# Performance work log

Measured on AMD Instinct MI355X. Metric: run time of the kernel, lower is better.

The kernel has to match this reference:

```python
import jax, jax.numpy as jnp
import numpy as np

HEADS = 16
DIM_HEAD = 64
DIM = 1024
INNER = HEADS * DIM_HEAD  # 1024
DIM_OUT = 1024


def setup_inputs() -> dict:
    key = jax.random.key(0)
    k1, k2, k3, k4 = jax.random.split(key, 4)
    B, N = 4, 2048
    x = jax.random.normal(k1, (B, N, DIM), dtype=jnp.float32)
    # hk.Linear(inner_dim*3, with_bias=False): weight shape [in, out]
    w_qkv = jax.random.normal(k2, (DIM, INNER * 3), dtype=jnp.float32) / np.sqrt(DIM)
    # hk.Linear(dim_out): weight [INNER, DIM_OUT] + bias
    w_out = jax.random.normal(k3, (INNER, DIM_OUT), dtype=jnp.float32) / np.sqrt(INNER)
    b_out = jax.random.normal(k4, (DIM_OUT,), dtype=jnp.float32) * 0.01
    return {"x": x, "w_qkv": w_qkv, "w_out": w_out, "b_out": b_out}


def reference(x, w_qkv, w_out, b_out):
    B, N, _ = x.shape
    scale = DIM_HEAD ** -0.5
    qkv = x @ w_qkv  # [B, N, 3*INNER]
    q, k, v = jnp.split(qkv, 3, axis=-1)
    # b n (h d) -> b h n d
    split_heads = lambda t: t.reshape(B, N, HEADS, DIM_HEAD).transpose(0, 2, 1, 3)
    q, k, v = split_heads(q), split_heads(k), split_heads(v)
    dots = jnp.einsum('bhid,bhjd->bhij', q, k) * scale  # [B, H, N, N]
    attn = jax.nn.softmax(dots, axis=-1)
    out = jnp.einsum('bhij,bhjd->bhid', attn, v)  # [B, H, N, D]
    out = out.transpose(0, 2, 1, 3).reshape(B, N, INNER)  # b h n d -> b n (h d)
    return out @ w_out + b_out
```

## Files before the change

kernel.cpp:

```cpp
#include <hip/hip_runtime.h>
#include <cstdint>


typedef unsigned short ushort_t;
typedef _Float16 half_t;
typedef half_t half8 __attribute__((ext_vector_type(8)));
typedef half_t half4 __attribute__((ext_vector_type(4)));
typedef __fp16 fp16x2 __attribute__((ext_vector_type(2)));
typedef float floatx4 __attribute__((ext_vector_type(4)));

#define QSCALE 0.18033688011112043f

__device__ __forceinline__ float bf2f(ushort_t h) {
  union { unsigned int u; float f; } v; v.u = ((unsigned int)h) << 16; return v.f;
}
__device__ __forceinline__ void async_copy16(const void* g, void* l) {
  __builtin_amdgcn_global_load_lds(
      reinterpret_cast<const __attribute__((address_space(1))) unsigned int*>(
          reinterpret_cast<uintptr_t>(g)),
      reinterpret_cast<__attribute__((address_space(3))) unsigned int*>(
          reinterpret_cast<uintptr_t>(l)),
      16, 0, 0);
}
__device__ __forceinline__ void lds_fence() {
  asm volatile("s_waitcnt lgkmcnt(0)" ::: "memory");
}
__device__ __forceinline__ void vm_fence() {
  asm volatile("s_waitcnt vmcnt(0)" ::: "memory");
}

__global__ __launch_bounds__(256) void detect_dtype(const ushort_t* __restrict__ x,
                                                    int* __restrict__ flag) {
  __shared__ int cnt;
  if (threadIdx.x == 0) cnt = 0;
  __syncthreads();
  int local = 0;
  for (int i = threadIdx.x; i < 8192; i += 256)
    if ((x[i] & 0x7F80u) == 0x7F80u) ++local;
  atomicAdd(&cnt, local);
  __syncthreads();
  if (threadIdx.x == 0) *flag = (cnt >= 2) ? 1 : 0;
}

__global__ __launch_bounds__(256) void convert_to_f16(const void* __restrict__ src,
                                                      half_t* __restrict__ dst, int n,
                                                      const int* __restrict__ flag) {
  const int i0 = (blockIdx.x * 256 + threadIdx.x) * 4;
  if (i0 >= n) return;
  if (*flag) {
    const float* s = (const float*)src;
#pragma unroll
    for (int j = 0; j < 4; ++j) dst[i0 + j] = (half_t)s[i0 + j];
  } else {
    const ushort_t* s = (const ushort_t*)src;
#pragma unroll
    for (int j = 0; j < 4; ++j) dst[i0 + j] = (half_t)bf2f(s[i0 + j]);
  }
}

__global__ __launch_bounds__(256) void convert_bias(const void* __restrict__ src,
                                                    float* __restrict__ dst,
                                                    const int* __restrict__ flag) {
  const int i = blockIdx.x * 256 + threadIdx.x;
  if (i >= 1024) return;
  dst[i] = (*flag) ? ((const float*)src)[i] : bf2f(((const ushort_t*)src)[i]);
}

__global__ __launch_bounds__(256) void transpose_conv2(const void* __restrict__ srcA,
                                                       half_t* __restrict__ dstA,
                                                       const void* __restrict__ srcB,
                                                       half_t* __restrict__ dstB,
                                                       const int* __restrict__ flag) {
  __shared__ half_t tile[64][65];
  const int bx = blockIdx.x;
  const void* src; half_t* dst; int C, c0;
  if (bx < 48) { src = srcA; dst = dstA; C = 3072; c0 = bx * 64; }
  else         { src = srcB; dst = dstB; C = 1024; c0 = (bx - 48) * 64; }
  const int R = 1024;
  const int r0 = blockIdx.y * 64;
  const int tx = threadIdx.x & 63, ty = threadIdx.x >> 6;
  if (*flag) {
    const float* s = (const float*)src;
    for (int i = ty; i < 64; i += 4) tile[i][tx] = (half_t)s[(size_t)(r0 + i) * C + (c0 + tx)];
  } else {
    const ushort_t* s = (const ushort_t*)src;
    for (int i = ty; i < 64; i += 4) tile[i][tx] = (half_t)bf2f(s[(size_t)(r0 + i) * C + (c0 + tx)]);
  }
  __syncthreads();
  for (int i = ty; i < 64; i += 4) dst[(size_t)(c0 + i) * R + (r0 + tx)] = tile[tx][i];
}

__global__ __launch_bounds__(256) void gemm_qkv_kernel(
    const half_t* __restrict__ X, const half_t* __restrict__ WT,
    half_t* __restrict__ Qb, half_t* __restrict__ Kb, half_t* __restrict__ VTb) {
  __shared__ half_t smem[128 * 136];
  half_t* As = smem;
  half_t* Bs = smem + 128 * 64;
  const int tid = threadIdx.x;
  const int wv = tid >> 6, lane = tid & 63;
  const int l15 = lane & 15, quad = lane >> 4;
  const int l7 = l15 & 7;
  const int wm = wv & 1, wn = wv >> 1;
  const int bid = blockIdx.x;
  const int xcd = bid & 7, idx = bid >> 3;
  const int mb = xcd * 8 + (idx & 7);
  const int nb = idx >> 3;
  const int rlo = lane >> 3, ci = lane & 7;
  const int sw_klo = (ci ^ rlo) * 8;

  floatx4 acc[4][4];
  const floatx4 z = {0.f, 0.f, 0.f, 0.f};
#pragma unroll
  for (int mi = 0; mi < 4; ++mi)
#pragma unroll
    for (int ni = 0; ni < 4; ++ni) acc[mi][ni] = z;

  const half_t* Abase = X + (size_t)mb * 128 * 1024;
  const half_t* Bbase = WT + (size_t)nb * 128 * 1024;

  for (int k0 = 0; k0 < 1024; k0 += 64) {
#pragma unroll
    for (int j = 0; j < 4; ++j) {
      const int rb = (wv * 4 + j) * 8;
      async_copy16(Abase + (size_t)(rb + rlo) * 1024 + k0 + sw_klo, &As[rb * 64]);
    }
#pragma unroll
    for (int j = 0; j < 4; ++j) {
      const int rb = (wv * 4 + j) * 8;
      async_copy16(Bbase + (size_t)(rb + rlo) * 1024 + k0 + sw_klo, &Bs[rb * 64]);
    }
    __syncthreads();
#pragma unroll
    for (int ks = 0; ks < 2; ++ks) {
      half8 af[4], bfv[4];
#pragma unroll
      for (int mi = 0; mi < 4; ++mi) {
        const int rr = wm * 64 + mi * 16 + l15;
        af[mi] = *(const half8*)&As[rr * 64 + (((ks * 4 + quad) ^ l7) * 8)];
      }
#pragma unroll
      for (int ni = 0; ni < 4; ++ni) {
        const int rr = wn * 64 + ni * 16 + l15;
        bfv[ni] = *(const half8*)&Bs[rr * 64 + (((ks * 4 + quad) ^ l7) * 8)];
      }
#pragma unroll
      for (int mi = 0; mi < 4; ++mi)
#pragma unroll
        for (int ni = 0; ni < 4; ++ni)
          acc[mi][ni] = __builtin_amdgcn_mfma_f32_16x16x32_f16(af[mi], bfv[ni], acc[mi][ni], 0, 0, 0);
    }
    __syncthreads();
  }

  const int which = nb >> 3;
  if (which != 2) {
    const float sc = (which == 0) ? QSCALE : 1.0f;
#pragma unroll
    for (int mi = 0; mi < 4; ++mi)
#pragma unroll
      for (int ni = 0; ni < 4; ++ni) {
        const int col = wn * 64 + ni * 16 + l15;
#pragma unroll
        for (int r = 0; r < 4; ++r) {
          const int row = wm * 64 + mi * 16 + quad * 4 + r;
          smem[row * 132 + col] = (half_t)(acc[mi][ni][r] * sc);
        }
      }
    __syncthreads();
    half_t* dstB = (which == 0) ? Qb : Kb;
    const int hbase = (nb & 7) * 2;
    const int c2 = lane * 2;
    const int hh = hbase + (c2 >> 6);
    const int dd = c2 & 63;
#pragma unroll 4
    for (int i = 0; i < 32; ++i) {
      const int row = wv * 32 + i;
      const uint32_t val = *(const uint32_t*)&smem[row * 132 + c2];
      const int rowg = mb * 128 + row;
      const int bb = rowg >> 11, nn = rowg & 2047;
      *(uint32_t*)&dstB[(((size_t)(bb * 16 + hh)) * 2048 + nn) * 64 + dd] = val;
    }
  } else {
    const int nb2 = nb - 16;
#pragma unroll
    for (int mi = 0; mi < 4; ++mi)
#pragma unroll
      for (int ni = 0; ni < 4; ++ni) {
        const int nl = wn * 64 + ni * 16 + l15;
#pragma unroll
        for (int r = 0; r < 4; ++r) {
          const int ml = wm * 64 + mi * 16 + quad * 4 + r;
          smem[nl * 136 + ml] = (half_t)acc[mi][ni][r];
        }
      }
    __syncthreads();
    const int bb = mb >> 4;
    const int nn0 = (mb * 128) & 2047;
    const int lane2 = lane * 2;
#pragma unroll 4
    for (int it = 0; it < 32; ++it) {
      const int row = it * 4 + wv;
      const int hh = nb2 * 2 + (row >> 6);
      const int dd = row & 63;
      const int keyoff = lane2 ^ ((dd & 8) ? 4 : 0);
      const uint32_t val = *(const uint32_t*)&smem[row * 136 + lane2];
      *(uint32_t*)&VTb[((size_t)((bb * 16 + hh) * 64 + dd)) * 2048 + nn0 + keyoff] = val;
    }
  }
}

__global__ __launch_bounds__(512) void attn_kernel(
    const half_t* __restrict__ Qb, const half_t* __restrict__ Kb,
    const half_t* __restrict__ VTb, half_t* __restrict__ Ob) {
  __shared__ half_t smem[16384];
  const int tid = threadIdx.x, wv = tid >> 6, lane = tid & 63;
  const int l15 = lane & 15, quad = lane >> 4;
  const int l7 = l15 & 7;
  const int bid = blockIdx.x;
  const int xcd = bid & 7, idx = bid >> 3;
  const int bh = ((idx & 7) << 3) + xcd;
  const int qt = idx >> 3;
  const int bq = bh >> 4, hh = bh & 15;
  const half_t* Qg = Qb + (size_t)bh * 2048 * 64;
  const half_t* Kg = Kb + (size_t)bh * 2048 * 64;
  const half_t* Vg = VTb + (size_t)bh * 64 * 2048;
  const int q0 = qt * 256;
  const int rlo = lane >> 3, ci = lane & 7;
  const int sw_klo = (ci ^ rlo) * 8;

  const int q1 = quad >> 1, qb0 = quad & 1, b3 = (l15 >> 3) & 1;
  int kx[2], vx[4];
#pragma unroll
  for (int ks = 0; ks < 2; ++ks) kx[ks] = ((ks * 4 + quad) ^ l7) * 8;
#pragma unroll
  for (int ki = 0; ki < 4; ++ki)
    vx[ki] = (((ki * 2 + q1) ^ l7) * 8) + ((qb0 ^ b3) * 4);

#pragma unroll
  for (int j = 0; j < 4; ++j) {
    const int rb = (wv * 4 + j) * 8;
    async_copy16(Qg + (size_t)(q0 + rb + rlo) * 64 + sw_klo, &smem[rb * 64]);
  }
  vm_fence();
  half8 aq[2][2];
#pragma unroll
  for (int ks = 0; ks < 2; ++ks)
#pragma unroll
    for (int qi = 0; qi < 2; ++qi) {
      const int rr = wv * 32 + qi * 16 + l15;
      aq[ks][qi] = *(const half8*)&smem[rr * 64 + (((ks * 4 + quad) ^ l7) * 8)];
    }
  __syncthreads();

  floatx4 o_acc[2][4];
  const floatx4 z = {0.f, 0.f, 0.f, 0.f};
  float l_st[2] = {0.f, 0.f};
#pragma unroll
  for (int qi = 0; qi < 2; ++qi)
#pragma unroll
    for (int di = 0; di < 4; ++di) o_acc[qi][di] = z;

  {
    const int rb = wv * 8;
    async_copy16(Kg + (size_t)(rb + rlo) * 64 + sw_klo, &smem[rb * 64]);
    async_copy16(Vg + (size_t)(rb + rlo) * 2048 + sw_klo, &smem[8192 + rb * 64]);
  }

#pragma unroll 2
  for (int t = 0; t < 32; ++t) {
    const int co = (t & 1) * 4096;
    const int po = 4096 - co;
    __syncthreads();
    if (t < 31) {
      const int rb = wv * 8;
      async_copy16(Kg + (size_t)((t + 1) * 64 + rb + rlo) * 64 + sw_klo,
                   &smem[po + rb * 64]);
      async_copy16(Vg + (size_t)(rb + rlo) * 2048 + (t + 1) * 64 + sw_klo,
                   &smem[8192 + po + rb * 64]);
    }
    const half_t* Kc = &smem[co];
    const half_t* Vc = &smem[8192 + co];

    floatx4 s_acc[4][2];
#pragma unroll
    for (int ki = 0; ki < 4; ++ki)
#pragma unroll
      for (int qi = 0; qi < 2; ++qi) s_acc[ki][qi] = z;
#pragma unroll
    for (int ks = 0; ks < 2; ++ks) {
      half8 bk[4];
#pragma unroll
      for (int ki = 0; ki < 4; ++ki)
        bk[ki] = *(const half8*)&Kc[(ki * 16 + l15) * 64 + kx[ks]];
      __builtin_amdgcn_s_setprio(1);
#pragma unroll
      for (int ki = 0; ki < 4; ++ki)
#pragma unroll
        for (int qi = 0; qi < 2; ++qi)
          s_acc[ki][qi] = __builtin_amdgcn_mfma_f32_16x16x32_f16(bk[ki], aq[ks][qi], s_acc[ki][qi], 0, 0, 0);
      __builtin_amdgcn_s_setprio(0);
    }

#pragma unroll
    for (int c = 0; c < 2; ++c) {
      half8 bv[4];
#pragma unroll
      for (int di = 0; di < 4; ++di) {
        union { half4 q[2]; half8 v; } b_;
        b_.q[0] = *(const half4*)&Vc[(di * 16 + l15) * 64 + vx[2 * c]];
        b_.q[1] = *(const half4*)&Vc[(di * 16 + l15) * 64 + vx[2 * c + 1]];
        bv[di] = b_.v;
      }
      union Ap { uint32_t u[4]; half8 h; } apu[2];
#pragma unroll
      for (int kii = 0; kii < 2; ++kii)
#pragma unroll
        for (int qi = 0; qi < 2; ++qi) {
          const int ki = c * 2 + kii;
          const float p0 = __builtin_amdgcn_exp2f(s_acc[ki][qi][0]);
          const float p1 = __builtin_amdgcn_exp2f(s_acc[ki][qi][1]);
          const float p2 = __builtin_amdgcn_exp2f(s_acc[ki][qi][2]);
          const float p3 = __builtin_amdgcn_exp2f(s_acc[ki][qi][3]);
          l_st[qi] += (p0 + p1) + (p2 + p3);
          union { fp16x2 v; uint32_t u; } lo_, hi_;
          lo_.v = __builtin_amdgcn_cvt_pkrtz(p0, p1);
          hi_.v = __builtin_amdgcn_cvt_pkrtz(p2, p3);
          apu[qi].u[kii * 2] = lo_.u;
          apu[qi].u[kii * 2 + 1] = hi_.u;
        }
      __builtin_amdgcn_s_setprio(1);
#pragma unroll
      for (int qi = 0; qi < 2; ++qi)
#pragma unroll
        for (int di = 0; di < 4; ++di)
          o_acc[qi][di] = __builtin_amdgcn_mfma_f32_16x16x32_f16(apu[qi].h, bv[di], o_acc[qi][di], 0, 0, 0);
      __builtin_amdgcn_s_setprio(0);
    }
  }

  float linv[2];
#pragma unroll
  for (int qi = 0; qi < 2; ++qi) {
    float rs = l_st[qi];
    rs += __shfl_xor(rs, 16);
    rs += __shfl_xor(rs, 32);
    linv[qi] = 1.0f / rs;
  }

  __syncthreads();
  const int c2 = (tid & 31) * 2;
  const int rbase = (tid >> 5) & 15;
#pragma unroll
  for (int p = 0; p < 2; ++p) {
    if ((wv >> 2) == p) {
      const int rw = (wv & 3) * 32;
#pragma unroll
      for (int qi = 0; qi < 2; ++qi)
#pragma unroll
        for (int r = 0; r < 4; ++r) {
          const float inv = __shfl(linv[qi], quad * 4 + r);
          const int rowl = rw + qi * 16 + quad * 4 + r;
#pragma unroll
          for (int di = 0; di < 4; ++di)
            smem[rowl * 72 + di * 16 + l15] = (half_t)(o_acc[qi][di][r] * inv);
        }
    }
    __syncthreads();
#pragma unroll 4
    for (int i = 0; i < 8; ++i) {
      const int rowl = i * 16 + rbase;
      const uint32_t val = *(const uint32_t*)&smem[rowl * 72 + c2];
      const int nn = q0 + p * 128 + rowl;
      *(uint32_t*)&Ob[((size_t)(bq * 2048 + nn)) * 1024 + hh * 64 + c2] = val;
    }
    __syncthreads();
  }
}

__global__ __launch_bounds__(256) void gemm_out_kernel(
    const half_t* __restrict__ A, const half_t* __restrict__ WT,
    const float* __restrict__ bias, float* __restrict__ out) {
  __shared__ half_t As[128 * 64];
  __shared__ half_t Bs[128 * 64];
  const int tid = threadIdx.x;
  const int wv = tid >> 6, lane = tid & 63;
  const int l15 = lane & 15, quad = lane >> 4;
  const int l7 = l15 & 7;
  const int wm = wv & 1, wn = wv >> 1;
  const int bid = blockIdx.x;
  const int xcd = bid & 7, idx = bid >> 3;
  const int mb = xcd * 8 + (idx & 7);
  const int nb = idx >> 3;
  const int rlo = lane >> 3, ci = lane & 7;
  const int sw_klo = (ci ^ rlo) * 8;

  floatx4 acc[4][4];
  const floatx4 z = {0.f, 0.f, 0.f, 0.f};
#pragma unroll
  for (int mi = 0; mi < 4; ++mi)
#pragma unroll
    for (int ni = 0; ni < 4; ++ni) acc[mi][ni] = z;

  const half_t* Abase = A + (size_t)mb * 128 * 1024;
  const half_t* Bbase = WT + (size_t)nb * 128 * 1024;

  for (int k0 = 0; k0 < 1024; k0 += 64) {
#pragma unroll
    for (int j = 0; j < 4; ++j) {
      const int rb = (wv * 4 + j) * 8;
      async_copy16(Abase + (size_t)(rb + rlo) * 1024 + k0 + sw_klo, &As[rb * 64]);
    }
#pragma unroll
    for (int j = 0; j < 4; ++j) {
      const int rb = (wv * 4 + j) * 8;
      async_copy16(Bbase + (size_t)(rb + rlo) * 1024 + k0 + sw_klo, &Bs[rb * 64]);
    }
    __syncthreads();
#pragma unroll
    for (int ks = 0; ks < 2; ++ks) {
      half8 af[4], bfv[4];
#pragma unroll
      for (int mi = 0; mi < 4; ++mi) {
        const int rr = wm * 64 + mi * 16 + l15;
        af[mi] = *(const half8*)&As[rr * 64 + (((ks * 4 + quad) ^ l7) * 8)];
      }
#pragma unroll
      for (int ni = 0; ni < 4; ++ni) {
        const int rr = wn * 64 + ni * 16 + l15;
        bfv[ni] = *(const half8*)&Bs[rr * 64 + (((ks * 4 + quad) ^ l7) * 8)];
      }
#pragma unroll
      for (int mi = 0; mi < 4; ++mi)
#pragma unroll
        for (int ni = 0; ni < 4; ++ni)
          acc[mi][ni] = __builtin_amdgcn_mfma_f32_16x16x32_f16(af[mi], bfv[ni], acc[mi][ni], 0, 0, 0);
    }
    __syncthreads();
  }

#pragma unroll
  for (int mi = 0; mi < 4; ++mi) {
#pragma unroll
    for (int ni = 0; ni < 4; ++ni) {
      const int colg = nb * 128 + wn * 64 + ni * 16 + l15;
      const float bs = bias[colg];
#pragma unroll
      for (int r = 0; r < 4; ++r) {
        const int rowg = mb * 128 + wm * 64 + mi * 16 + quad * 4 + r;
        out[(size_t)rowg * 1024 + colg] = acc[mi][ni][r] + bs;
      }
    }
  }
}

extern "C" void kernel_launch(void* const* d_in, const int* in_sizes, int n_in,
                              void* d_out, int out_size, void* d_ws, size_t ws_size,
                              hipStream_t stream) {
  const void* x_raw     = d_in[0];
  const void* w_qkv_raw = d_in[1];
  const void* w_out_raw = d_in[2];
  const void* b_out_raw = d_in[3];
  float* out = (float*)d_out;

  char* ws = (char*)d_ws;
  half_t* xb    = (half_t*)(ws);
  half_t* Qb    = (half_t*)(ws + ((size_t)16 << 20));
  half_t* Kb    = (half_t*)(ws + ((size_t)32 << 20));
  half_t* VTb   = (half_t*)(ws + ((size_t)48 << 20));
  half_t* WTqkv = (half_t*)(ws + ((size_t)64 << 20));
  half_t* WTout = (half_t*)(ws + ((size_t)70 << 20));
  float*  bb    = (float*)(ws + ((size_t)72 << 20));
  int*    flag  = (int*)(ws + ((size_t)72 << 20) + 8192);
  half_t* Ob    = xb;

  detect_dtype<<<1, 256, 0, stream>>>((const ushort_t*)x_raw, flag);
  convert_to_f16<<<8192, 256, 0, stream>>>(x_raw, xb, 8192 * 1024, flag);
  convert_bias<<<4, 256, 0, stream>>>(b_out_raw, bb, flag);
  transpose_conv2<<<dim3(64, 16), 256, 0, stream>>>(w_qkv_raw, WTqkv, w_out_raw, WTout, flag);
  gemm_qkv_kernel<<<1536, 256, 0, stream>>>(xb, WTqkv, Qb, Kb, VTb);
  attn_kernel<<<512, 512, 0, stream>>>(Qb, Kb, VTb, Ob);
  gemm_out_kernel<<<512, 256, 0, stream>>>(Ob, WTout, bb, out);
}
```

Baseline: 277.8 us.

## Use four-stage K/V LDS ring and process two tiles per barrier

Grows shared memory to hold four K/V tile buffers and restructures the main attention loop so each iteration processes two 64-key tiles after a single barrier, while prefetching the next two tiles. This halves the number of block-wide barriers and gives async loads more lead time to hide global latency. LDS use doubles to 64 KB per block, which may reduce occupancy. The scores still use exp2 with no running max, so the numerics are unchanged.

```diff
diff --git a/kernel.cpp b/kernel.cpp
--- a/kernel.cpp
+++ b/kernel.cpp
@@ -212,7 +212,7 @@
 __global__ __launch_bounds__(512) void attn_kernel(
     const half_t* __restrict__ Qb, const half_t* __restrict__ Kb,
     const half_t* __restrict__ VTb, half_t* __restrict__ Ob) {
-  __shared__ half_t smem[16384];
+  __shared__ half_t smem[32768];
   const int tid = threadIdx.x, wv = tid >> 6, lane = tid & 63;
   const int l15 = lane & 15, quad = lane >> 4;
   const int l7 = l15 & 7;
@@ -262,79 +262,91 @@
 
   {
     const int rb = wv * 8;
-    async_copy16(Kg + (size_t)(rb + rlo) * 64 + sw_klo, &smem[rb * 64]);
-    async_copy16(Vg + (size_t)(rb + rlo) * 2048 + sw_klo, &smem[8192 + rb * 64]);
+#pragma unroll
+    for (int u = 0; u < 2; ++u) {
+      async_copy16(Kg + (size_t)(u * 64 + rb + rlo) * 64 + sw_klo,
+                   &smem[u * 4096 + rb * 64]);
+      async_copy16(Vg + (size_t)(rb + rlo) * 2048 + u * 64 + sw_klo,
+                   &smem[16384 + u * 4096 + rb * 64]);
+    }
   }
 
 #pragma unroll 2
-  for (int t = 0; t < 32; ++t) {
-    const int co = (t & 1) * 4096;
-    const int po = 4096 - co;
-    __syncthreads();
-    if (t < 31) {
+  for (int t = 0; t < 32; t += 2) {
+    __syncthreads();
+    if (t < 30) {
       const int rb = wv * 8;
-      async_copy16(Kg + (size_t)((t + 1) * 64 + rb + rlo) * 64 + sw_klo,
-                   &smem[po + rb * 64]);
-      async_copy16(Vg + (size_t)(rb + rlo) * 2048 + (t + 1) * 64 + sw_klo,
-                   &smem[8192 + po + rb * 64]);
-    }
-    const half_t* Kc = &smem[co];
-    const half_t* Vc = &smem[8192 + co];
-
-    floatx4 s_acc[4][2];
-#pragma unroll
-    for (int ki = 0; ki < 4; ++ki)
-#pragma unroll
-      for (int qi = 0; qi < 2; ++qi) s_acc[ki][qi] = z;
-#pragma unroll
-    for (int ks = 0; ks < 2; ++ks) {
-      half8 bk[4];
+#pragma unroll
+      for (int u = 2; u < 4; ++u) {
+        const int tp = t + u;
+        const int buf = tp & 3;
+        async_copy16(Kg + (size_t)(tp * 64 + rb + rlo) * 64 + sw_klo,
+                     &smem[buf * 4096 + rb * 64]);
+        async_copy16(Vg + (size_t)(rb + rlo) * 2048 + tp * 64 + sw_klo,
+                     &smem[16384 + buf * 4096 + rb * 64]);
+      }
+    }
+#pragma unroll
+    for (int u = 0; u < 2; ++u) {
+      const int buf = (t + u) & 3;
+      const half_t* Kc = &smem[buf * 4096];
+      const half_t* Vc = &smem[16384 + buf * 4096];
+
+      floatx4 s_acc[4][2];
 #pragma unroll
       for (int ki = 0; ki < 4; ++ki)
-        bk[ki] = *(const half8*)&Kc[(ki * 16 + l15) * 64 + kx[ks]];
-      __builtin_amdgcn_s_setprio(1);
-#pragma unroll
-      for (int ki = 0; ki < 4; ++ki)
+#pragma unroll
+        for (int qi = 0; qi < 2; ++qi) s_acc[ki][qi] = z;
+#pragma unroll
+      for (int ks = 0; ks < 2; ++ks) {
+        half8 bk[4];
+#pragma unroll
+        for (int ki = 0; ki < 4; ++ki)
+          bk[ki] = *(const half8*)&Kc[(ki * 16 + l15) * 64 + kx[ks]];
+        __builtin_amdgcn_s_setprio(1);
+#pragma unroll
+        for (int ki = 0; ki < 4; ++ki)
+#pragma unroll
+          for (int qi = 0; qi < 2; ++qi)
+            s_acc[ki][qi] = __builtin_amdgcn_mfma_f32_16x16x32_f16(bk[ki], aq[ks][qi], s_acc[ki][qi], 0, 0, 0);
+        __builtin_amdgcn_s_setprio(0);
+      }
+
+#pragma unroll
+      for (int c = 0; c < 2; ++c) {
+        half8 bv[4];
+#pragma unroll
+        for (int di = 0; di < 4; ++di) {
+          union { half4 q[2]; half8 v; } b_;
+          b_.q[0] = *(const half4*)&Vc[(di * 16 + l15) * 64 + vx[2 * c]];
+          b_.q[1] = *(const half4*)&Vc[(di * 16 + l15) * 64 + vx[2 * c + 1]];
+          bv[di] = b_.v;
+        }
+        union Ap { uint32_t u[4]; half8 h; } apu[2];
+#pragma unroll
+        for (int kii = 0; kii < 2; ++kii)
+#pragma unroll
+          for (int qi = 0; qi < 2; ++qi) {
+            const int ki = c * 2 + kii;
+            const float p0 = __builtin_amdgcn_exp2f(s_acc[ki][qi][0]);
+            const float p1 = __builtin_amdgcn_exp2f(s_acc[ki][qi][1]);
+            const float p2 = __builtin_amdgcn_exp2f(s_acc[ki][qi][2]);
+            const float p3 = __builtin_amdgcn_exp2f(s_acc[ki][qi][3]);
+            l_st[qi] += (p0 + p1) + (p2 + p3);
+            union { fp16x2 v; uint32_t u; } lo_, hi_;
+            lo_.v = __builtin_amdgcn_cvt_pkrtz(p0, p1);
+            hi_.v = __builtin_amdgcn_cvt_pkrtz(p2, p3);
+            apu[qi].u[kii * 2] = lo_.u;
+            apu[qi].u[kii * 2 + 1] = hi_.u;
+          }
+        __builtin_amdgcn_s_setprio(1);
 #pragma unroll
         for (int qi = 0; qi < 2; ++qi)
-          s_acc[ki][qi] = __builtin_amdgcn_mfma_f32_16x16x32_f16(bk[ki], aq[ks][qi], s_acc[ki][qi], 0, 0, 0);
-      __builtin_amdgcn_s_setprio(0);
-    }
-
-#pragma unroll
-    for (int c = 0; c < 2; ++c) {
-      half8 bv[4];
-#pragma unroll
-      for (int di = 0; di < 4; ++di) {
-        union { half4 q[2]; half8 v; } b_;
-        b_.q[0] = *(const half4*)&Vc[(di * 16 + l15) * 64 + vx[2 * c]];
-        b_.q[1] = *(const half4*)&Vc[(di * 16 + l15) * 64 + vx[2 * c + 1]];
-        bv[di] = b_.v;
-      }
-      union Ap { uint32_t u[4]; half8 h; } apu[2];
-#pragma unroll
-      for (int kii = 0; kii < 2; ++kii)
-#pragma unroll
-        for (int qi = 0; qi < 2; ++qi) {
-          const int ki = c * 2 + kii;
-          const float p0 = __builtin_amdgcn_exp2f(s_acc[ki][qi][0]);
-          const float p1 = __builtin_amdgcn_exp2f(s_acc[ki][qi][1]);
-          const float p2 = __builtin_amdgcn_exp2f(s_acc[ki][qi][2]);
-          const float p3 = __builtin_amdgcn_exp2f(s_acc[ki][qi][3]);
-          l_st[qi] += (p0 + p1) + (p2 + p3);
-          union { fp16x2 v; uint32_t u; } lo_, hi_;
-          lo_.v = __builtin_amdgcn_cvt_pkrtz(p0, p1);
-          hi_.v = __builtin_amdgcn_cvt_pkrtz(p2, p3);
-          apu[qi].u[kii * 2] = lo_.u;
-          apu[qi].u[kii * 2 + 1] = hi_.u;
-        }
-      __builtin_amdgcn_s_setprio(1);
-#pragma unroll
-      for (int qi = 0; qi < 2; ++qi)
-#pragma unroll
-        for (int di = 0; di < 4; ++di)
-          o_acc[qi][di] = __builtin_amdgcn_mfma_f32_16x16x32_f16(apu[qi].h, bv[di], o_acc[qi][di], 0, 0, 0);
-      __builtin_amdgcn_s_setprio(0);
+#pragma unroll
+          for (int di = 0; di < 4; ++di)
+            o_acc[qi][di] = __builtin_amdgcn_mfma_f32_16x16x32_f16(apu[qi].h, bv[di], o_acc[qi][di], 0, 0, 0);
+        __builtin_amdgcn_s_setprio(0);
+      }
     }
   }
 
```

Measured after the change: 272.2 us. 1.02x faster.
